# Kernel tuning notes

Measured on AMD Instinct MI355X. Metric: run time of the kernel, lower is better.

Reference implementation:

```python
import jax, jax.numpy as jnp
import numpy as np

B, T, D_IN = 32, 1000, 1024
H = 32          # hidden_size
G = 4 * H       # gate dim (i,f,g,o)
L = 4           # num_layers


def setup_inputs() -> dict:
    key = jax.random.key(0)
    ks = jax.random.split(key, 12)
    s = 1.0 / np.sqrt(H)  # PyTorch LSTM init scale
    inp = {
        'x': jax.random.normal(ks[0], (B, T, D_IN), dtype=jnp.float32),
        # layer 0 (input dim 1024), [dir, ...]
        'w_ih0': jax.random.uniform(ks[1], (2, G, D_IN), minval=-s, maxval=s),
        'w_hh0': jax.random.uniform(ks[2], (2, G, H), minval=-s, maxval=s),
        'b_ih0': jax.random.uniform(ks[3], (2, G), minval=-s, maxval=s),
        'b_hh0': jax.random.uniform(ks[4], (2, G), minval=-s, maxval=s),
        # layers 1..3 (input dim 2H=64), [layer, dir, ...]
        'w_ih': jax.random.uniform(ks[5], (L - 1, 2, G, 2 * H), minval=-s, maxval=s),
        'w_hh': jax.random.uniform(ks[6], (L - 1, 2, G, H), minval=-s, maxval=s),
        'b_ih': jax.random.uniform(ks[7], (L - 1, 2, G), minval=-s, maxval=s),
        'b_hh': jax.random.uniform(ks[8], (L - 1, 2, G), minval=-s, maxval=s),
        # fc: Linear(64, 1)
        'fc_w': jax.random.uniform(ks[9], (1, 2 * H), minval=-0.125, maxval=0.125),
        'fc_b': jax.random.uniform(ks[10], (1,), minval=-0.125, maxval=0.125),
    }
    return inp


def _lstm_dir(x, wi, wh, b, reverse):
    # x: [B,T,Din]; wi: [4H,Din]; wh: [4H,H]; b: [4H]
    xp = jnp.einsum('btd,gd->tbg', x, wi) + b  # precomputed input proj [T,B,4H]
    whT = wh.T

    def step(carry, xt):
        h, c = carry
        g = xt + h @ whT
        i, f, gg, o = jnp.split(g, 4, axis=-1)  # PyTorch gate order i,f,g,o
        c = jax.nn.sigmoid(f) * c + jax.nn.sigmoid(i) * jnp.tanh(gg)
        h = jax.nn.sigmoid(o) * jnp.tanh(c)
        return (h, c), h

    init = (jnp.zeros((x.shape[0], H), x.dtype), jnp.zeros((x.shape[0], H), x.dtype))
    _, hs = jax.lax.scan(step, init, xp, reverse=reverse)  # hs aligned with input time order
    return hs.transpose(1, 0, 2)  # [B,T,H]


def _bilstm(x, wi, wh, bi, bh):
    fwd = _lstm_dir(x, wi[0], wh[0], bi[0] + bh[0], False)
    bwd = _lstm_dir(x, wi[1], wh[1], bi[1] + bh[1], True)
    return jnp.concatenate([fwd, bwd], axis=-1)  # [B,T,2H]


def reference(x, w_ih0, w_hh0, b_ih0, b_hh0, w_ih, w_hh, b_ih, b_hh, fc_w, fc_b):
    h = _bilstm(x, w_ih0, w_hh0, b_ih0, b_hh0)
    for l in range(L - 1):
        h = _bilstm(h, w_ih[l], w_hh[l], b_ih[l], b_hh[l])
    pooled = h.mean(axis=-2)           # [B,2H]
    return pooled @ fc_w.T + fc_b      # [B,1]
```

## Files before the change

kernel.cpp:

```cpp
#include <hip/hip_runtime.h>


#define TB 1000
#define LOG2E 1.44269504088896340736f

typedef int   v2i __attribute__((ext_vector_type(2)));
typedef float v2f __attribute__((ext_vector_type(2)));

__device__ __forceinline__ float fexp2(float x) {
#if __has_builtin(__builtin_amdgcn_exp2f)
    return __builtin_amdgcn_exp2f(x);
#else
    return exp2f(x);
#endif
}

__device__ __forceinline__ float lane_xor32(float v, bool pickx) {
    v2i r = __builtin_amdgcn_permlane32_swap(__float_as_int(v), __float_as_int(v),
                                             false, false);
    return __int_as_float(pickx ? r[0] : r[1]);
}

__global__ __launch_bounds__(256)
void gemm_proj(const float* __restrict__ A, int K,
               const float* __restrict__ W,
               const float* __restrict__ bi,
               const float* __restrict__ bh,
               float* __restrict__ xpT)
{
    __shared__ __align__(16) float As[32][132];
    __shared__ __align__(16) float Bs[32][132];

    const int tid = threadIdx.x;
    const int m0 = blockIdx.x * 128;
    const int n0 = blockIdx.y * 128;
    const int tx = tid & 15;
    const int ty = tid >> 4;

    float acc[8][8];
#pragma unroll
    for (int i = 0; i < 8; ++i)
#pragma unroll
        for (int jj = 0; jj < 8; ++jj) acc[i][jj] = 0.0f;

    const int ar = tid >> 1;
    const int ak = (tid & 1) * 16;

    for (int k0 = 0; k0 < K; k0 += 32) {
        const float* ap = A + (size_t)(m0 + ar) * K + k0 + ak;
        float4 a0 = *(const float4*)(ap + 0);
        float4 a1 = *(const float4*)(ap + 4);
        float4 a2 = *(const float4*)(ap + 8);
        float4 a3 = *(const float4*)(ap + 12);
        const float* wp = W + (size_t)(n0 + ar) * K + k0 + ak;
        float4 w0 = *(const float4*)(wp + 0);
        float4 w1 = *(const float4*)(wp + 4);
        float4 w2 = *(const float4*)(wp + 8);
        float4 w3 = *(const float4*)(wp + 12);

        __syncthreads();
        {
            float av_[16] = {a0.x, a0.y, a0.z, a0.w, a1.x, a1.y, a1.z, a1.w,
                             a2.x, a2.y, a2.z, a2.w, a3.x, a3.y, a3.z, a3.w};
#pragma unroll
            for (int q = 0; q < 16; ++q) As[ak + q][ar] = av_[q];
            float wv_[16] = {w0.x, w0.y, w0.z, w0.w, w1.x, w1.y, w1.z, w1.w,
                             w2.x, w2.y, w2.z, w2.w, w3.x, w3.y, w3.z, w3.w};
#pragma unroll
            for (int q = 0; q < 16; ++q) Bs[ak + q][ar] = wv_[q];
        }
        __syncthreads();

#pragma unroll
        for (int kk = 0; kk < 32; ++kk) {
            float4 av0 = *(const float4*)&As[kk][tx * 8];
            float4 av1 = *(const float4*)&As[kk][tx * 8 + 4];
            float4 bv0 = *(const float4*)&Bs[kk][ty * 8];
            float4 bv1 = *(const float4*)&Bs[kk][ty * 8 + 4];
            float am[8] = {av0.x, av0.y, av0.z, av0.w, av1.x, av1.y, av1.z, av1.w};
            float wn[8] = {bv0.x, bv0.y, bv0.z, bv0.w, bv1.x, bv1.y, bv1.z, bv1.w};
#pragma unroll
            for (int ni = 0; ni < 8; ++ni)
#pragma unroll
                for (int mi = 0; mi < 8; ++mi)
                    acc[ni][mi] = fmaf(am[mi], wn[ni], acc[ni][mi]);
        }
    }

    const int dir = n0 >> 7;
    const int mbase = m0 + tx * 8;
#pragma unroll
    for (int ni = 0; ni < 8; ++ni) {
        const int n = n0 + ty * 8 + ni;
        const float bias = bi[n] + bh[n];
        const float sc = (((n >> 5) & 3) == 2) ? (-2.0f * LOG2E) : (-LOG2E);
        float* rowp = xpT + ((size_t)(dir * 32 * 128) + (n & 127)) * TB;
#pragma unroll
        for (int qd = 0; qd < 2; ++qd) {
            const int mq = mbase + qd * 4;
            const int bidx = mq / 1000;
            const int ttq = mq - bidx * 1000;
            float* rp = rowp + (size_t)bidx * 128 * TB;
            if (dir == 0) {
                float4 o = {(acc[ni][qd*4+0] + bias) * sc,
                            (acc[ni][qd*4+1] + bias) * sc,
                            (acc[ni][qd*4+2] + bias) * sc,
                            (acc[ni][qd*4+3] + bias) * sc};
                *(float4*)(rp + ttq) = o;
            } else {
                float4 o = {(acc[ni][qd*4+3] + bias) * sc,
                            (acc[ni][qd*4+2] + bias) * sc,
                            (acc[ni][qd*4+1] + bias) * sc,
                            (acc[ni][qd*4+0] + bias) * sc};
                *(float4*)(rp + (TB - 4 - ttq)) = o;
            }
        }
    }
}

template<int MODE>
__global__ __launch_bounds__(64)
void lstm_rec(const float* __restrict__ xpT,
              const float* __restrict__ whh,
              float* __restrict__ hout,
              float* __restrict__ hsum)
{
    __shared__ __align__(16) float hsh[32];

    const int blk  = blockIdx.x;
    const int dir  = blk >> 5;
    const int b    = blk & 31;
    const int lane = threadIdx.x & 63;
    const int j    = lane & 31;
    const int up   = lane >> 5;
    const int r0   = j + up * 64;
    const int r1   = r0 + 32;

    v2i det = __builtin_amdgcn_permlane32_swap(lane, lane, false, false);
    const bool pickx = (det[0] == (lane ^ 32));

    const float sA = up ? (-2.0f * LOG2E) : (-LOG2E);
    const float sB = -LOG2E;
    v2f wa[16], wb[16];
    {
        const float* wp0 = whh + (size_t)(dir * 128 + r0) * 32;
        const float* wp1 = whh + (size_t)(dir * 128 + r1) * 32;
#pragma unroll
        for (int q = 0; q < 8; ++q) {
            float4 v = *(const float4*)(wp0 + q * 4);
            wa[2 * q + 0][0] = v.x * sA; wa[2 * q + 0][1] = v.y * sA;
            wa[2 * q + 1][0] = v.z * sA; wa[2 * q + 1][1] = v.w * sA;
            float4 u = *(const float4*)(wp1 + q * 4);
            wb[2 * q + 0][0] = u.x * sB; wb[2 * q + 0][1] = u.y * sB;
            wb[2 * q + 1][0] = u.z * sB; wb[2 * q + 1][1] = u.w * sB;
        }
    }

    const float* pa = xpT + ((size_t)blk * 128 + r0) * TB;
    const float* pb = xpT + ((size_t)blk * 128 + r1) * TB;

    float4 A0 = *(const float4*)(pa + 0);
    float4 B0 = *(const float4*)(pb + 0);
    float4 A1 = *(const float4*)(pa + 4);
    float4 B1 = *(const float4*)(pb + 4);

    const float mA = up ?  2.0f : 1.0f;
    const float mB = up ? -1.0f : 0.0f;

    float cs = 0.0f, h = 0.0f, hacc = 0.0f;
    float* hq = hout + ((size_t)b * TB + (dir ? TB - 1 : 0)) * 64 + dir * 32 + j;
    const int hstep = dir ? -64 : 64;

    const unsigned lds_z  = (unsigned)(size_t)&hsh[0];
    const unsigned lds_wa = lds_z + 4u * (unsigned)j;

    float4 hv0, hv1, hv2, hv3, hv4v, hv5, hv6, hv7;

#define DS_WRITE_H() \
    asm volatile("ds_write_b32 %0, %1" :: "v"(lds_wa), "v"(h))

#define DS_ISSUE_READS() do {                                                   \
    asm volatile("ds_read_b128 %0, %1 offset:0"   : "=v"(hv0)  : "v"(lds_z));   \
    asm volatile("ds_read_b128 %0, %1 offset:16"  : "=v"(hv1)  : "v"(lds_z));   \
    asm volatile("ds_read_b128 %0, %1 offset:32"  : "=v"(hv2)  : "v"(lds_z));   \
    asm volatile("ds_read_b128 %0, %1 offset:48"  : "=v"(hv3)  : "v"(lds_z));   \
    asm volatile("ds_read_b128 %0, %1 offset:64"  : "=v"(hv4v) : "v"(lds_z));   \
    asm volatile("ds_read_b128 %0, %1 offset:80"  : "=v"(hv5)  : "v"(lds_z));   \
    asm volatile("ds_read_b128 %0, %1 offset:96"  : "=v"(hv6)  : "v"(lds_z));   \
    asm volatile("ds_read_b128 %0, %1 offset:112" : "=v"(hv7)  : "v"(lds_z));   \
    } while (0)

#define MVG(HV, CNT, I0, I1, Q)                                                 \
    asm volatile("s_waitcnt lgkmcnt(" #CNT ")");                                \
    __builtin_amdgcn_sched_barrier(0);                                          \
    {                                                                           \
        v2f h0_ = {HV.x, HV.y};                                                 \
        v2f h1_ = {HV.z, HV.w};                                                 \
        qa[I0] = __builtin_elementwise_fma(h0_, wa[2*Q],   qa[I0]);             \
        qb[I0] = __builtin_elementwise_fma(h0_, wb[2*Q],   qb[I0]);             \
        qa[I1] = __builtin_elementwise_fma(h1_, wa[2*Q+1], qa[I1]);             \
        qb[I1] = __builtin_elementwise_fma(h1_, wb[2*Q+1], qb[I1]);             \
    }

    DS_WRITE_H();
    DS_ISSUE_READS();

#define LSTM_STEP(GA, GB) do {                                                  \
        v2f qa[4], qb[4];                                                       \
        qa[0] = v2f{(GA), 0.0f}; qa[1] = v2f{0.f, 0.f};                         \
        qa[2] = v2f{0.f, 0.f};   qa[3] = v2f{0.f, 0.f};                         \
        qb[0] = v2f{(GB), 0.0f}; qb[1] = v2f{0.f, 0.f};                         \
        qb[2] = v2f{0.f, 0.f};   qb[3] = v2f{0.f, 0.f};                         \
        MVG(hv0,  7, 0, 1, 0)                                                   \
        MVG(hv1,  6, 2, 3, 1)                                                   \
        MVG(hv2,  5, 0, 1, 2)                                                   \
        MVG(hv3,  4, 2, 3, 3)                                                   \
        MVG(hv4v, 3, 0, 1, 4)                                                   \
        MVG(hv5,  2, 2, 3, 5)                                                   \
        MVG(hv6,  1, 0, 1, 6)                                                   \
        MVG(hv7,  0, 2, 3, 7)                                                   \
        v2f sa = (qa[0] + qa[2]) + (qa[1] + qa[3]);                             \
        v2f sb = (qb[0] + qb[2]) + (qb[1] + qb[3]);                             \
        float g0 = sa[0] + sa[1];                                               \
        float g1 = sb[0] + sb[1];                                               \
        float s0 = __builtin_amdgcn_rcpf(1.0f + fexp2(g0));                     \
        float v0 = fmaf(mA, s0, mB);               \
        float v1 = __builtin_amdgcn_rcpf(1.0f + fexp2(g1));  \
        float o0 = lane_xor32(v0, pickx);                                       \
        float o1 = lane_xor32(v1, pickx);                                       \
        float P  = v0 * o0;                        \
        float Ps = P * (-2.0f * LOG2E);                                         \
        float sf = up ? o1 : v1;                                                \
        float so = up ? v1 : o1;                                                \
        cs = fmaf(sf, cs, Ps);                            \
        float r_ = __builtin_amdgcn_rcpf(1.0f + fexp2(cs));                     \
        float so2 = so + so;                                                    \
        h = fmaf(so2, r_, -so);                             \
        DS_WRITE_H();                                                           \
        DS_ISSUE_READS();                                                       \
        if (MODE == 0) {                                                        \
            asm volatile("global_store_dword %0, %1, off" :: "v"(hq), "v"(h));  \
        } else {                                                                \
            hacc += h;                                                          \
        }                                                                       \
        hq += hstep;                                                            \
    } while (0)

    for (int it = 0; it < 125; ++it) {
        const int base = it * 8;
        const int offn0 = min(base + 8,  TB - 4);
        const int offn1 = min(base + 12, TB - 4);
        float4 NA0 = *(const float4*)(pa + offn0);
        float4 NB0 = *(const float4*)(pb + offn0);
        float4 NA1 = *(const float4*)(pa + offn1);
        float4 NB1 = *(const float4*)(pb + offn1);

        LSTM_STEP(A0.x, B0.x);
        LSTM_STEP(A0.y, B0.y);
        LSTM_STEP(A0.z, B0.z);
        LSTM_STEP(A0.w, B0.w);
        LSTM_STEP(A1.x, B1.x);
        LSTM_STEP(A1.y, B1.y);
        LSTM_STEP(A1.z, B1.z);
        LSTM_STEP(A1.w, B1.w);

        A0 = NA0; B0 = NB0; A1 = NA1; B1 = NB1;
    }
#undef LSTM_STEP
#undef MVG
#undef DS_ISSUE_READS
#undef DS_WRITE_H

    asm volatile("s_waitcnt lgkmcnt(0)" ::: "memory");

    if (MODE == 1) hsum[b * 64 + dir * 32 + j] = hacc;
}

__global__ __launch_bounds__(64)
void final_fc(const float* __restrict__ hsum,
              const float* __restrict__ fcw,
              const float* __restrict__ fcb,
              float* __restrict__ out)
{
    int b = blockIdx.x;
    int l = threadIdx.x;
    float v = hsum[b * 64 + l] * (1.0f / (float)TB) * fcw[l];
#pragma unroll
    for (int off = 32; off > 0; off >>= 1)
        v += __shfl_down(v, off, 64);
    if (l == 0) out[b] = v + fcb[0];
}

extern "C" void kernel_launch(void* const* d_in, const int* in_sizes, int n_in,
                              void* d_out, int out_size, void* d_ws, size_t ws_size,
                              hipStream_t stream)
{
    const float* x    = (const float*)d_in[0];
    const float* wih0 = (const float*)d_in[1];
    const float* whh0 = (const float*)d_in[2];
    const float* bih0 = (const float*)d_in[3];
    const float* bhh0 = (const float*)d_in[4];
    const float* wih  = (const float*)d_in[5];
    const float* whh  = (const float*)d_in[6];
    const float* bih  = (const float*)d_in[7];
    const float* bhh  = (const float*)d_in[8];
    const float* fcw  = (const float*)d_in[9];
    const float* fcb  = (const float*)d_in[10];
    float* out = (float*)d_out;

    float* ws = (float*)d_ws;
    float* xp = ws;
    float* hb = ws + 8192000;
    float* hs = ws + 8192000 + 2048000;

    dim3 gb(250, 2);

    gemm_proj<<<gb, 256, 0, stream>>>(x, 1024, wih0, bih0, bhh0, xp);
    lstm_rec<0><<<64, 64, 0, stream>>>(xp, whh0, hb, hs);

    for (int l = 1; l < 4; ++l) {
        const float* wl  = wih + (size_t)(l - 1) * 2 * 128 * 64;
        const float* whl = whh + (size_t)(l - 1) * 2 * 128 * 32;
        const float* b1  = bih + (size_t)(l - 1) * 256;
        const float* b2  = bhh + (size_t)(l - 1) * 256;
        gemm_proj<<<gb, 256, 0, stream>>>(hb, 64, wl, b1, b2, xp);
        if (l == 3) lstm_rec<1><<<64, 64, 0, stream>>>(xp, whl, hb, hs);
        else        lstm_rec<0><<<64, 64, 0, stream>>>(xp, whl, hb, hs);
    }

    final_fc<<<32, 64, 0, stream>>>(hs, fcw, fcb, out);
}
```

Baseline: 1.021 ms.

## Interleave forward and backward LSTM chains in one wavefront per batch

The recurrent kernel now runs both directions for a batch element in a single 64-thread block, interleaving the two independent recurrence chains so each chain's latency can be hidden behind the other. It replaces the hand-scheduled inline-asm LDS reads and writes with plain shared-memory accesses, and halves the grid from 64 to 32 blocks. The GEMM's A-tile read pattern is also changed to strided float4 reads to reduce LDS bank conflicts. The interleaving doubles register use for weights and removes the careful waitcnt pipelining. The plain LDS write followed by reads within a single wavefront relies on in-order LDS behaviour.

Result: slower. 1.987 ms (+94.6%).

```diff
diff --git a/kernel.cpp b/kernel.cpp
--- a/kernel.cpp
+++ b/kernel.cpp
@@ -73,8 +73,8 @@
 
 #pragma unroll
         for (int kk = 0; kk < 32; ++kk) {
-            float4 av0 = *(const float4*)&As[kk][tx * 8];
-            float4 av1 = *(const float4*)&As[kk][tx * 8 + 4];
+            float4 av0 = *(const float4*)&As[kk][tx * 4];
+            float4 av1 = *(const float4*)&As[kk][64 + tx * 4];
             float4 bv0 = *(const float4*)&Bs[kk][ty * 8];
             float4 bv1 = *(const float4*)&Bs[kk][ty * 8 + 4];
             float am[8] = {av0.x, av0.y, av0.z, av0.w, av1.x, av1.y, av1.z, av1.w};
@@ -88,7 +88,6 @@
     }
 
     const int dir = n0 >> 7;
-    const int mbase = m0 + tx * 8;
 #pragma unroll
     for (int ni = 0; ni < 8; ++ni) {
         const int n = n0 + ty * 8 + ni;
@@ -97,7 +96,7 @@
         float* rowp = xpT + ((size_t)(dir * 32 * 128) + (n & 127)) * TB;
 #pragma unroll
         for (int qd = 0; qd < 2; ++qd) {
-            const int mq = mbase + qd * 4;
+            const int mq = m0 + qd * 64 + tx * 4;
             const int bidx = mq / 1000;
             const int ttq = mq - bidx * 1000;
             float* rp = rowp + (size_t)bidx * 128 * TB;
@@ -119,17 +118,16 @@
 }
 
 template<int MODE>
-__global__ __launch_bounds__(64)
+__global__ __launch_bounds__(64, 1)
 void lstm_rec(const float* __restrict__ xpT,
               const float* __restrict__ whh,
               float* __restrict__ hout,
               float* __restrict__ hsum)
 {
-    __shared__ __align__(16) float hsh[32];
-
-    const int blk  = blockIdx.x;
-    const int dir  = blk >> 5;
-    const int b    = blk & 31;
+    __shared__ __align__(16) float hsh0[32];
+    __shared__ __align__(16) float hsh1[32];
+
+    const int b    = blockIdx.x;
     const int lane = threadIdx.x & 63;
     const int j    = lane & 31;
     const int up   = lane >> 5;
@@ -141,86 +139,73 @@
 
     const float sA = up ? (-2.0f * LOG2E) : (-LOG2E);
     const float sB = -LOG2E;
-    v2f wa[16], wb[16];
-    {
-        const float* wp0 = whh + (size_t)(dir * 128 + r0) * 32;
-        const float* wp1 = whh + (size_t)(dir * 128 + r1) * 32;
+
+    v2f wa0[16], wb0[16], wa1[16], wb1[16];
+#pragma unroll
+    for (int d = 0; d < 2; ++d) {
+        const float* wp0 = whh + (size_t)(d * 128 + r0) * 32;
+        const float* wp1 = whh + (size_t)(d * 128 + r1) * 32;
+        v2f* WA = d ? wa1 : wa0;
+        v2f* WB = d ? wb1 : wb0;
 #pragma unroll
         for (int q = 0; q < 8; ++q) {
             float4 v = *(const float4*)(wp0 + q * 4);
-            wa[2 * q + 0][0] = v.x * sA; wa[2 * q + 0][1] = v.y * sA;
-            wa[2 * q + 1][0] = v.z * sA; wa[2 * q + 1][1] = v.w * sA;
+            WA[2 * q + 0][0] = v.x * sA; WA[2 * q + 0][1] = v.y * sA;
+            WA[2 * q + 1][0] = v.z * sA; WA[2 * q + 1][1] = v.w * sA;
             float4 u = *(const float4*)(wp1 + q * 4);
-            wb[2 * q + 0][0] = u.x * sB; wb[2 * q + 0][1] = u.y * sB;
-            wb[2 * q + 1][0] = u.z * sB; wb[2 * q + 1][1] = u.w * sB;
+            WB[2 * q + 0][0] = u.x * sB; WB[2 * q + 0][1] = u.y * sB;
+            WB[2 * q + 1][0] = u.z * sB; WB[2 * q + 1][1] = u.w * sB;
         }
     }
 
-    const float* pa = xpT + ((size_t)blk * 128 + r0) * TB;
-    const float* pb = xpT + ((size_t)blk * 128 + r1) * TB;
-
-    float4 A0 = *(const float4*)(pa + 0);
-    float4 B0 = *(const float4*)(pb + 0);
-    float4 A1 = *(const float4*)(pa + 4);
-    float4 B1 = *(const float4*)(pb + 4);
+    const float* pa0 = xpT + ((size_t)b * 128 + r0) * TB;
+    const float* pb0 = xpT + ((size_t)b * 128 + r1) * TB;
+    const float* pa1 = xpT + ((size_t)(32 + b) * 128 + r0) * TB;
+    const float* pb1 = xpT + ((size_t)(32 + b) * 128 + r1) * TB;
+
+    float4 A0_0 = *(const float4*)(pa0 + 0);
+    float4 B0_0 = *(const float4*)(pb0 + 0);
+    float4 A1_0 = *(const float4*)(pa0 + 4);
+    float4 B1_0 = *(const float4*)(pb0 + 4);
+    float4 A0_1 = *(const float4*)(pa1 + 0);
+    float4 B0_1 = *(const float4*)(pb1 + 0);
+    float4 A1_1 = *(const float4*)(pa1 + 4);
+    float4 B1_1 = *(const float4*)(pb1 + 4);
 
     const float mA = up ?  2.0f : 1.0f;
     const float mB = up ? -1.0f : 0.0f;
 
-    float cs = 0.0f, h = 0.0f, hacc = 0.0f;
-    float* hq = hout + ((size_t)b * TB + (dir ? TB - 1 : 0)) * 64 + dir * 32 + j;
-    const int hstep = dir ? -64 : 64;
-
-    const unsigned lds_z  = (unsigned)(size_t)&hsh[0];
-    const unsigned lds_wa = lds_z + 4u * (unsigned)j;
-
-    float4 hv0, hv1, hv2, hv3, hv4v, hv5, hv6, hv7;
-
-#define DS_WRITE_H() \
-    asm volatile("ds_write_b32 %0, %1" :: "v"(lds_wa), "v"(h))
-
-#define DS_ISSUE_READS() do {                                                   \
-    asm volatile("ds_read_b128 %0, %1 offset:0"   : "=v"(hv0)  : "v"(lds_z));   \
-    asm volatile("ds_read_b128 %0, %1 offset:16"  : "=v"(hv1)  : "v"(lds_z));   \
-    asm volatile("ds_read_b128 %0, %1 offset:32"  : "=v"(hv2)  : "v"(lds_z));   \
-    asm volatile("ds_read_b128 %0, %1 offset:48"  : "=v"(hv3)  : "v"(lds_z));   \
-    asm volatile("ds_read_b128 %0, %1 offset:64"  : "=v"(hv4v) : "v"(lds_z));   \
-    asm volatile("ds_read_b128 %0, %1 offset:80"  : "=v"(hv5)  : "v"(lds_z));   \
-    asm volatile("ds_read_b128 %0, %1 offset:96"  : "=v"(hv6)  : "v"(lds_z));   \
-    asm volatile("ds_read_b128 %0, %1 offset:112" : "=v"(hv7)  : "v"(lds_z));   \
-    } while (0)
-
-#define MVG(HV, CNT, I0, I1, Q)                                                 \
-    asm volatile("s_waitcnt lgkmcnt(" #CNT ")");                                \
-    __builtin_amdgcn_sched_barrier(0);                                          \
-    {                                                                           \
-        v2f h0_ = {HV.x, HV.y};                                                 \
-        v2f h1_ = {HV.z, HV.w};                                                 \
-        qa[I0] = __builtin_elementwise_fma(h0_, wa[2*Q],   qa[I0]);             \
-        qb[I0] = __builtin_elementwise_fma(h0_, wb[2*Q],   qb[I0]);             \
-        qa[I1] = __builtin_elementwise_fma(h1_, wa[2*Q+1], qa[I1]);             \
-        qb[I1] = __builtin_elementwise_fma(h1_, wb[2*Q+1], qb[I1]);             \
-    }
-
-    DS_WRITE_H();
-    DS_ISSUE_READS();
-
-#define LSTM_STEP(GA, GB) do {                                                  \
-        v2f qa[4], qb[4];                                                       \
-        qa[0] = v2f{(GA), 0.0f}; qa[1] = v2f{0.f, 0.f};                         \
-        qa[2] = v2f{0.f, 0.f};   qa[3] = v2f{0.f, 0.f};                         \
-        qb[0] = v2f{(GB), 0.0f}; qb[1] = v2f{0.f, 0.f};                         \
-        qb[2] = v2f{0.f, 0.f};   qb[3] = v2f{0.f, 0.f};                         \
-        MVG(hv0,  7, 0, 1, 0)                                                   \
-        MVG(hv1,  6, 2, 3, 1)                                                   \
-        MVG(hv2,  5, 0, 1, 2)                                                   \
-        MVG(hv3,  4, 2, 3, 3)                                                   \
-        MVG(hv4v, 3, 0, 1, 4)                                                   \
-        MVG(hv5,  2, 2, 3, 5)                                                   \
-        MVG(hv6,  1, 0, 1, 6)                                                   \
-        MVG(hv7,  0, 2, 3, 7)                                                   \
-        v2f sa = (qa[0] + qa[2]) + (qa[1] + qa[3]);                             \
-        v2f sb = (qb[0] + qb[2]) + (qb[1] + qb[3]);                             \
+    float cs0 = 0.0f, h0 = 0.0f, hacc0 = 0.0f;
+    float cs1 = 0.0f, h1 = 0.0f, hacc1 = 0.0f;
+    float* hq0 = hout + ((size_t)b * TB) * 64 + j;
+    float* hq1 = hout + ((size_t)b * TB + TB - 1) * 64 + 32 + j;
+
+    hsh0[j] = 0.0f;
+    hsh1[j] = 0.0f;
+
+#define CHAIN_STEP(HS, WA, WB, CS, H, HQ, HSTEP, HACC, GA, GB) do {             \
+        v2f hv[16];                                                             \
+        _Pragma("unroll")                                                       \
+        for (int q = 0; q < 8; ++q) {                                           \
+            float4 t = *(const float4*)&HS[q * 4];                              \
+            hv[2 * q + 0][0] = t.x; hv[2 * q + 0][1] = t.y;                     \
+            hv[2 * q + 1][0] = t.z; hv[2 * q + 1][1] = t.w;                     \
+        }                                                                       \
+        v2f qa0 = {(GA), 0.0f}, qa1 = {0.f,0.f}, qa2 = {0.f,0.f}, qa3 = {0.f,0.f}; \
+        v2f qb0 = {(GB), 0.0f}, qb1 = {0.f,0.f}, qb2 = {0.f,0.f}, qb3 = {0.f,0.f}; \
+        _Pragma("unroll")                                                       \
+        for (int q = 0; q < 4; ++q) {                                           \
+            qa0 = __builtin_elementwise_fma(hv[4*q+0], WA[4*q+0], qa0);         \
+            qb0 = __builtin_elementwise_fma(hv[4*q+0], WB[4*q+0], qb0);         \
+            qa1 = __builtin_elementwise_fma(hv[4*q+1], WA[4*q+1], qa1);         \
+            qb1 = __builtin_elementwise_fma(hv[4*q+1], WB[4*q+1], qb1);         \
+            qa2 = __builtin_elementwise_fma(hv[4*q+2], WA[4*q+2], qa2);         \
+            qb2 = __builtin_elementwise_fma(hv[4*q+2], WB[4*q+2], qb2);         \
+            qa3 = __builtin_elementwise_fma(hv[4*q+3], WA[4*q+3], qa3);         \
+            qb3 = __builtin_elementwise_fma(hv[4*q+3], WB[4*q+3], qb3);         \
+        }                                                                       \
+        v2f sa = (qa0 + qa1) + (qa2 + qa3);                                     \
+        v2f sb = (qb0 + qb1) + (qb2 + qb3);                                     \
         float g0 = sa[0] + sa[1];                                               \
         float g1 = sb[0] + sb[1];                                               \
         float s0 = __builtin_amdgcn_rcpf(1.0f + fexp2(g0));                     \
@@ -232,48 +217,51 @@
         float Ps = P * (-2.0f * LOG2E);                                         \
         float sf = up ? o1 : v1;                                                \
         float so = up ? v1 : o1;                                                \
-        cs = fmaf(sf, cs, Ps);                            \
-        float r_ = __builtin_amdgcn_rcpf(1.0f + fexp2(cs));                     \
+        CS = fmaf(sf, CS, Ps);                            \
+        float r_ = __builtin_amdgcn_rcpf(1.0f + fexp2(CS));                     \
         float so2 = so + so;                                                    \
-        h = fmaf(so2, r_, -so);                             \
-        DS_WRITE_H();                                                           \
-        DS_ISSUE_READS();                                                       \
-        if (MODE == 0) {                                                        \
-            asm volatile("global_store_dword %0, %1, off" :: "v"(hq), "v"(h));  \
-        } else {                                                                \
-            hacc += h;                                                          \
-        }                                                                       \
-        hq += hstep;                                                            \
+        H = fmaf(so2, r_, -so);                             \
+        HS[j] = H;                                                              \
+        if (MODE == 0) *HQ = H; else HACC += H;                                 \
+        HQ += HSTEP;                                                            \
     } while (0)
+
+#define STEP2(S0A, S0B, S1A, S1B)                                               \
+    CHAIN_STEP(hsh0, wa0, wb0, cs0, h0, hq0,  64, hacc0, S0A, S0B);             \
+    CHAIN_STEP(hsh1, wa1, wb1, cs1, h1, hq1, -64, hacc1, S1A, S1B);
 
     for (int it = 0; it < 125; ++it) {
         const int base = it * 8;
         const int offn0 = min(base + 8,  TB - 4);
         const int offn1 = min(base + 12, TB - 4);
-        float4 NA0 = *(const float4*)(pa + offn0);
-        float4 NB0 = *(const float4*)(pb + offn0);
-        float4 NA1 = *(const float4*)(pa + offn1);
-        float4 NB1 = *(const float4*)(pb + offn1);
-
-        LSTM_STEP(A0.x, B0.x);
-        LSTM_STEP(A0.y, B0.y);
-        LSTM_STEP(A0.z, B0.z);
-        LSTM_STEP(A0.w, B0.w);
-        LSTM_STEP(A1.x, B1.x);
-        LSTM_STEP(A1.y, B1.y);
-        LSTM_STEP(A1.z, B1.z);
-        LSTM_STEP(A1.w, B1.w);
-
-        A0 = NA0; B0 = NB0; A1 = NA1; B1 = NB1;
-    }
-#undef LSTM_STEP
-#undef MVG
-#undef DS_ISSUE_READS
-#undef DS_WRITE_H
-
-    asm volatile("s_waitcnt lgkmcnt(0)" ::: "memory");
-
-    if (MODE == 1) hsum[b * 64 + dir * 32 + j] = hacc;
+        float4 NA0_0 = *(const float4*)(pa0 + offn0);
+        float4 NB0_0 = *(const float4*)(pb0 + offn0);
+        float4 NA1_0 = *(const float4*)(pa0 + offn1);
+        float4 NB1_0 = *(const float4*)(pb0 + offn1);
+        float4 NA0_1 = *(const float4*)(pa1 + offn0);
+        float4 NB0_1 = *(const float4*)(pb1 + offn0);
+        float4 NA1_1 = *(const float4*)(pa1 + offn1);
+        float4 NB1_1 = *(const float4*)(pb1 + offn1);
+
+        STEP2(A0_0.x, B0_0.x, A0_1.x, B0_1.x);
+        STEP2(A0_0.y, B0_0.y, A0_1.y, B0_1.y);
+        STEP2(A0_0.z, B0_0.z, A0_1.z, B0_1.z);
+        STEP2(A0_0.w, B0_0.w, A0_1.w, B0_1.w);
+        STEP2(A1_0.x, B1_0.x, A1_1.x, B1_1.x);
+        STEP2(A1_0.y, B1_0.y, A1_1.y, B1_1.y);
+        STEP2(A1_0.z, B1_0.z, A1_1.z, B1_1.z);
+        STEP2(A1_0.w, B1_0.w, A1_1.w, B1_1.w);
+
+        A0_0 = NA0_0; B0_0 = NB0_0; A1_0 = NA1_0; B1_0 = NB1_0;
+        A0_1 = NA0_1; B0_1 = NB0_1; A1_1 = NA1_1; B1_1 = NB1_1;
+    }
+#undef STEP2
+#undef CHAIN_STEP
+
+    if (MODE == 1) {
+        hsum[b * 64 + j]      = hacc0;
+        hsum[b * 64 + 32 + j] = hacc1;
+    }
 }
 
 __global__ __launch_bounds__(64)
@@ -316,7 +304,7 @@
     dim3 gb(250, 2);
 
     gemm_proj<<<gb, 256, 0, stream>>>(x, 1024, wih0, bih0, bhh0, xp);
-    lstm_rec<0><<<64, 64, 0, stream>>>(xp, whh0, hb, hs);
+    lstm_rec<0><<<32, 64, 0, stream>>>(xp, whh0, hb, hs);
 
     for (int l = 1; l < 4; ++l) {
         const float* wl  = wih + (size_t)(l - 1) * 2 * 128 * 64;
@@ -324,8 +312,8 @@
         const float* b1  = bih + (size_t)(l - 1) * 256;
         const float* b2  = bhh + (size_t)(l - 1) * 256;
         gemm_proj<<<gb, 256, 0, stream>>>(hb, 64, wl, b1, b2, xp);
-        if (l == 3) lstm_rec<1><<<64, 64, 0, stream>>>(xp, whl, hb, hs);
-        else        lstm_rec<0><<<64, 64, 0, stream>>>(xp, whl, hb, hs);
+        if (l == 3) lstm_rec<1><<<32, 64, 0, stream>>>(xp, whl, hb, hs);
+        else        lstm_rec<0><<<32, 64, 0, stream>>>(xp, whl, hb, hs);
     }
 
     final_fc<<<32, 64, 0, stream>>>(hs, fcw, fcb, out);
```
